# Optimization experiments

Measured on AMD Instinct MI355X. Metric: run time of the kernel, lower is better.

## Reference

```python
import jax, jax.numpy as jnp
import numpy as np
import math

PHI = (1 + math.sqrt(5)) / 2
COMPRESS_EXP = 2.0 / 3.0
ALPHA_D = 0.01


def c_mag(z):
    return jnp.sqrt(z[..., 0] ** 2 + z[..., 1] ** 2 + 1e-08)


def c_phase(z):
    return jnp.arctan2(z[..., 1], z[..., 0] + 1e-10)


def c_mul(a, b):
    real = a[..., 0] * b[..., 0] - a[..., 1] * b[..., 1]
    imag = a[..., 0] * b[..., 1] + a[..., 1] * b[..., 0]
    return jnp.stack([real, imag], axis=-1)


@jax.custom_vjp
def fractal_compress(mag):
    return jnp.clip(mag, 1e-08) ** COMPRESS_EXP


def _fc_fwd(mag):
    ms = jnp.clip(mag, 1e-08)
    c = ms ** COMPRESS_EXP
    return c, c / (ms + 1e-06)


def _fc_bwd(ratio, g):
    return (g * jnp.minimum(ratio, 2.0),)


fractal_compress.defvjp(_fc_fwd, _fc_bwd)


def converge(z):
    mag = c_mag(z)
    phase = c_phase(z)
    cm = fractal_compress(mag)
    return jnp.stack([cm * jnp.cos(phase), cm * jnp.sin(phase)], axis=-1)


def setup_inputs():
    key = jax.random.key(0)
    Bsz, T, D, S = 4, 512, 1024, 16
    dt_rank = D // 16
    ks = jax.random.split(key, 8)
    scale = 1.0 / PHI

    def u(k, shape):
        fan_in = shape[1]
        lim = scale / math.sqrt(fan_in)
        return jax.random.uniform(k, shape, minval=-lim, maxval=lim, dtype=jnp.float32)

    return {
        "x": jax.random.normal(ks[0], (Bsz, T, D), dtype=jnp.float32),
        "W_in": u(ks[1], (2 * D, D)),
        "W_xproj": u(ks[2], (dt_rank + 4 * S, D)),
        "W_dt": u(ks[3], (D, dt_rank)),
        "b_dt": jax.random.uniform(ks[4], (D,), minval=-0.1, maxval=0.1, dtype=jnp.float32),
        "W_out": u(ks[5], (D, D)),
        "b_out": jax.random.uniform(ks[6], (D,), minval=-0.1, maxval=0.1, dtype=jnp.float32),
        "W_res": u(ks[7], (2 * S, D)),
        "A_log": jnp.log(jnp.linspace(1.0, float(S), S)),
    }


def reference(x, W_in, W_xproj, W_dt, b_dt, W_out, b_out, W_res, A_log):
    Bsz, T, D = x.shape
    S = A_log.shape[0]
    dt_rank = W_dt.shape[1]

    xz = x @ W_in.T                      # [B,T,2D]
    x_in, z = xz[..., :D], xz[..., D:]
    x_in = jax.nn.silu(x_in)
    xp = x_in @ W_xproj.T                # [B,T,dt_rank+4S]
    dt = jax.nn.softplus(xp[..., :dt_rank] @ W_dt.T + b_dt)   # [B,T,D]
    bc = xp[..., dt_rank:].reshape(Bsz, T, 2, S, 2)
    B_all, C_all = bc[:, :, 0], bc[:, :, 1]                    # [B,T,S,2]

    A_neg = -jnp.exp(A_log)              # [S]

    # initial deep state d: differentiated phases, tiny magnitude
    phases = jnp.linspace(0.0, 2 * math.pi * (1 - 1.0 / S), S)
    d0 = jnp.stack([0.01 * jnp.cos(phases), 0.01 * jnp.sin(phases)], axis=-1)
    d0 = jnp.broadcast_to(d0, (Bsz, S, 2)).astype(x.dtype)
    h0 = jnp.zeros((Bsz, D, S, 2), dtype=x.dtype)

    def step(carry, xs):
        h_prev, d_prev = carry
        x_t, dt_t, B_t, C_t = xs        # [B,D], [B,D], [B,S,2], [B,S,2]
        x_complex = (x_t @ W_res.T).reshape(Bsz, S, 2)
        d_read = jax.lax.stop_gradient(d_prev)
        T_gate = jnp.cos((c_phase(x_complex) - c_phase(d_read)) / 2) ** 2  # [B,S]
        d_mag = c_mag(d_read)[..., None]
        d_normed = d_read / (d_mag + 1e-08)
        d_scale = jnp.sqrt(jnp.clip(d_mag, 1e-06, 20.0))
        surfaced = d_normed * d_scale * T_gate[..., None]                  # [B,S,2]

        alpha = jnp.exp(dt_t[..., None] * A_neg)                           # [B,D,S]
        x_full = jnp.stack([x_t, jnp.zeros_like(x_t)], axis=-1)            # [B,D,2]
        Bx = c_mul(B_t[:, None, :, :], x_full[:, :, None, :])              # [B,D,S,2]
        Bx = Bx + surfaced[:, None, :, :]
        Bx = Bx * dt_t[:, :, None, None]                                   # gamma scaling

        h_decayed = h_prev * alpha[..., None]
        released = h_prev * (1.0 - alpha)[..., None]
        comp = jnp.clip(converge(released), -10.0, 10.0)
        comp_avg = comp.mean(axis=1)                                       # [B,S,2]
        d_t = jax.lax.stop_gradient(d_prev) + ALPHA_D * comp_avg
        d_mag_new = c_mag(d_t)[..., None]
        d_t = jnp.where(d_mag_new > 20.0, d_t * (20.0 / d_mag_new), d_t)

        h_t = h_decayed + Bx
        Ch = c_mul(C_t[:, None, :, :], h_t)                                # [B,D,S,2]
        y_t = Ch[..., 0].sum(axis=-1)                                      # [B,D]
        return (h_t, d_t), y_t

    xs = (
        jnp.swapaxes(x_in, 0, 1),
        jnp.swapaxes(dt, 0, 1),
        jnp.swapaxes(B_all, 0, 1),
        jnp.swapaxes(C_all, 0, 1),
    )
    (_, _), ys = jax.lax.scan(step, (h0, d0), xs)
    y = jnp.swapaxes(ys, 0, 1)           # [B,T,D]
    y = y * jax.nn.silu(z)
    return y @ W_out.T + b_out
```

## Files before the change

kernel.cpp:

```cpp
#include <hip/hip_runtime.h>
#include <hip/hip_bf16.h>
#include <math.h>


enum { EPI_NONE=0, EPI_SILU=1, EPI_SPBIAS=2, EPI_BIAS=3 };

template<int EPI>
__device__ __forceinline__ float epi_apply(float v, float b) {
  if constexpr (EPI == EPI_SILU)        { return v / (1.0f + expf(-v)); }
  else if constexpr (EPI == EPI_SPBIAS) { float t = v + b; return fmaxf(t, 0.0f) + log1pf(expf(-fabsf(t))); }
  else if constexpr (EPI == EPI_BIAS)   { return v + b; }
  else return v;
}

template<int EPI, bool HAS_A2>
__global__ __launch_bounds__(256) void gemm_wt(
    const float* __restrict__ A, int lda,
    const float* __restrict__ A2, int lda2,
    const float* __restrict__ W, int ldw,
    const float* __restrict__ bias,
    float* __restrict__ C, int ldc,
    int N, int K)
{
  constexpr int BM = 64, BN = 64, BK = 16, PAD = 4;
  __shared__ float As[BK][BM + PAD];
  __shared__ float Ws[BK][BN + PAD];
  const int m0 = blockIdx.x * BM;
  const int n0 = blockIdx.y * BN;
  const int tid = threadIdx.x;
  const int tx = tid & 15;
  const int ty = tid >> 4;
  const int lm = tid >> 2;
  const int lk = (tid & 3) << 2;

  float acc[4][4] = {{0.f,0.f,0.f,0.f},{0.f,0.f,0.f,0.f},{0.f,0.f,0.f,0.f},{0.f,0.f,0.f,0.f}};

  for (int k0 = 0; k0 < K; k0 += BK) {
    float4 av, wv;
    {
      const float* p = A + (size_t)(m0 + lm) * lda + k0 + lk;
      av = *(const float4*)p;
      if (HAS_A2) {
        const float4 a2 = *(const float4*)(A2 + (size_t)(m0 + lm) * lda2 + k0 + lk);
        av.x *= a2.x; av.y *= a2.y; av.z *= a2.z; av.w *= a2.w;
      }
    }
    {
      const int n = n0 + lm;
      if (n < N) wv = *(const float4*)(W + (size_t)n * ldw + k0 + lk);
      else       wv = make_float4(0.f, 0.f, 0.f, 0.f);
    }
    __syncthreads();
    As[lk+0][lm] = av.x; As[lk+1][lm] = av.y; As[lk+2][lm] = av.z; As[lk+3][lm] = av.w;
    Ws[lk+0][lm] = wv.x; Ws[lk+1][lm] = wv.y; Ws[lk+2][lm] = wv.z; Ws[lk+3][lm] = wv.w;
    __syncthreads();
#pragma unroll
    for (int kk = 0; kk < BK; ++kk) {
      const float4 a = *(const float4*)&As[kk][ty << 2];
      const float4 w = *(const float4*)&Ws[kk][tx << 2];
      const float ar[4] = {a.x, a.y, a.z, a.w};
      const float wr[4] = {w.x, w.y, w.z, w.w};
#pragma unroll
      for (int i = 0; i < 4; ++i)
#pragma unroll
        for (int j = 0; j < 4; ++j)
          acc[i][j] = fmaf(ar[i], wr[j], acc[i][j]);
    }
  }

  const int ncol = n0 + (tx << 2);
  float bj[4] = {0.f, 0.f, 0.f, 0.f};
  if constexpr (EPI == EPI_SPBIAS || EPI == EPI_BIAS) {
    if (ncol < N) { const float4 bv = *(const float4*)(bias + ncol); bj[0]=bv.x; bj[1]=bv.y; bj[2]=bv.z; bj[3]=bv.w; }
  }
  if (ncol < N) {
#pragma unroll
    for (int i = 0; i < 4; ++i) {
      float vs[4];
#pragma unroll
      for (int j = 0; j < 4; ++j) vs[j] = epi_apply<EPI>(acc[i][j], bj[j]);
      *(float4*)(C + (size_t)(m0 + (ty << 2) + i) * ldc + ncol) = make_float4(vs[0], vs[1], vs[2], vs[3]);
    }
  }
}

__global__ __launch_bounds__(256) void gemm_dualw(
    const float* __restrict__ A, int lda,
    const float* __restrict__ W1,
    const float* __restrict__ W2, int ldw,
    float* __restrict__ C, int ldc,
    int N, int K)
{
  constexpr int BM = 64, BN = 64, BK = 16, PAD = 4;
  __shared__ float As[BK][BM + PAD];
  __shared__ float Ws[BK][BN + PAD];
  const int m0 = blockIdx.x * BM;
  const int n0 = blockIdx.y * BN;
  const int tid = threadIdx.x;
  const int tx = tid & 15;
  const int ty = tid >> 4;
  const int lm = tid >> 2;
  const int lk = (tid & 3) << 2;

  float acc[4][4] = {{0.f,0.f,0.f,0.f},{0.f,0.f,0.f,0.f},{0.f,0.f,0.f,0.f},{0.f,0.f,0.f,0.f}};

  for (int k0 = 0; k0 < K; k0 += BK) {
    float4 av, wv;
    av = *(const float4*)(A + (size_t)(m0 + lm) * lda + k0 + lk);
    {
      const int n = n0 + lm;
      if (n < N) {
        const float* wp = (n < 128) ? (W1 + (size_t)n * ldw + k0 + lk)
                                    : (W2 + (size_t)(n - 128) * ldw + k0 + lk);
        wv = *(const float4*)wp;
      } else wv = make_float4(0.f, 0.f, 0.f, 0.f);
    }
    __syncthreads();
    As[lk+0][lm] = av.x; As[lk+1][lm] = av.y; As[lk+2][lm] = av.z; As[lk+3][lm] = av.w;
    Ws[lk+0][lm] = wv.x; Ws[lk+1][lm] = wv.y; Ws[lk+2][lm] = wv.z; Ws[lk+3][lm] = wv.w;
    __syncthreads();
#pragma unroll
    for (int kk = 0; kk < BK; ++kk) {
      const float4 a = *(const float4*)&As[kk][ty << 2];
      const float4 w = *(const float4*)&Ws[kk][tx << 2];
      const float ar[4] = {a.x, a.y, a.z, a.w};
      const float wr[4] = {w.x, w.y, w.z, w.w};
#pragma unroll
      for (int i = 0; i < 4; ++i)
#pragma unroll
        for (int j = 0; j < 4; ++j)
          acc[i][j] = fmaf(ar[i], wr[j], acc[i][j]);
    }
  }

  const int ncol = n0 + (tx << 2);
  if (ncol < N) {
#pragma unroll
    for (int i = 0; i < 4; ++i)
      *(float4*)(C + (size_t)(m0 + (ty << 2) + i) * ldc + ncol) =
          make_float4(acc[i][0], acc[i][1], acc[i][2], acc[i][3]);
  }
}

template<int EPI>
__global__ __launch_bounds__(256) void gemm_128x64(
    const float* __restrict__ A, int lda,
    const float* __restrict__ W, int ldw,
    float* __restrict__ C, int ldc, int K)
{
  constexpr int BM = 128, BN = 64, BK = 16, PAD = 4;
  __shared__ float As[BK][BM + PAD];
  __shared__ float Ws[BK][BN + PAD];
  const int m0 = blockIdx.x * BM;
  const int n0 = blockIdx.y * BN;
  const int tid = threadIdx.x;
  const int tx = tid & 15;
  const int ty = tid >> 4;
  const int lmA = tid >> 1;
  const int lkA = (tid & 1) << 3;
  const int lmW = tid >> 2;
  const int lkW = (tid & 3) << 2;

  float acc[8][4];
#pragma unroll
  for (int i = 0; i < 8; ++i)
#pragma unroll
    for (int j = 0; j < 4; ++j) acc[i][j] = 0.f;

  for (int k0 = 0; k0 < K; k0 += BK) {
    const float* pa = A + (size_t)(m0 + lmA) * lda + k0 + lkA;
    const float4 a0 = ((const float4*)pa)[0];
    const float4 a1 = ((const float4*)pa)[1];
    const float4 wv = *(const float4*)(W + (size_t)(n0 + lmW) * ldw + k0 + lkW);
    __syncthreads();
    As[lkA+0][lmA]=a0.x; As[lkA+1][lmA]=a0.y; As[lkA+2][lmA]=a0.z; As[lkA+3][lmA]=a0.w;
    As[lkA+4][lmA]=a1.x; As[lkA+5][lmA]=a1.y; As[lkA+6][lmA]=a1.z; As[lkA+7][lmA]=a1.w;
    Ws[lkW+0][lmW]=wv.x; Ws[lkW+1][lmW]=wv.y; Ws[lkW+2][lmW]=wv.z; Ws[lkW+3][lmW]=wv.w;
    __syncthreads();
#pragma unroll
    for (int kk = 0; kk < BK; ++kk) {
      const float4 x0 = *(const float4*)&As[kk][ty << 3];
      const float4 x1 = *(const float4*)&As[kk][(ty << 3) + 4];
      const float4 w  = *(const float4*)&Ws[kk][tx << 2];
      const float ar[8] = {x0.x,x0.y,x0.z,x0.w,x1.x,x1.y,x1.z,x1.w};
      const float wr[4] = {w.x,w.y,w.z,w.w};
#pragma unroll
      for (int i = 0; i < 8; ++i)
#pragma unroll
        for (int j = 0; j < 4; ++j)
          acc[i][j] = fmaf(ar[i], wr[j], acc[i][j]);
    }
  }

  const int ncol = n0 + (tx << 2);
#pragma unroll
  for (int i = 0; i < 8; ++i) {
    float vs[4];
#pragma unroll
    for (int j = 0; j < 4; ++j) vs[j] = epi_apply<EPI>(acc[i][j], 0.f);
    *(float4*)(C + (size_t)(m0 + (ty << 3) + i) * ldc + ncol) = make_float4(vs[0], vs[1], vs[2], vs[3]);
  }
}

__global__ __launch_bounds__(256) void gemm_dt64(
    const float* __restrict__ A, int lda,
    const float* __restrict__ W,
    const float* __restrict__ bias,
    float* __restrict__ C, int ldc)
{
  __shared__ float As[64][68];
  __shared__ float Ws[64][68];
  const int m0 = blockIdx.x * 64;
  const int n0 = blockIdx.y * 64;
  const int tid = threadIdx.x;
  const int lm = tid & 63;
  const int kq = (tid >> 6) << 4;

  {
    const float* pa = A + (size_t)(m0 + lm) * lda + kq;
    const float4 a0 = ((const float4*)pa)[0];
    const float4 a1 = ((const float4*)pa)[1];
    const float4 a2 = ((const float4*)pa)[2];
    const float4 a3 = ((const float4*)pa)[3];
    const float* pw = W + (size_t)(n0 + lm) * 64 + kq;
    const float4 w0 = ((const float4*)pw)[0];
    const float4 w1 = ((const float4*)pw)[1];
    const float4 w2 = ((const float4*)pw)[2];
    const float4 w3 = ((const float4*)pw)[3];
    As[kq+ 0][lm]=a0.x; As[kq+ 1][lm]=a0.y; As[kq+ 2][lm]=a0.z; As[kq+ 3][lm]=a0.w;
    As[kq+ 4][lm]=a1.x; As[kq+ 5][lm]=a1.y; As[kq+ 6][lm]=a1.z; As[kq+ 7][lm]=a1.w;
    As[kq+ 8][lm]=a2.x; As[kq+ 9][lm]=a2.y; As[kq+10][lm]=a2.z; As[kq+11][lm]=a2.w;
    As[kq+12][lm]=a3.x; As[kq+13][lm]=a3.y; As[kq+14][lm]=a3.z; As[kq+15][lm]=a3.w;
    Ws[kq+ 0][lm]=w0.x; Ws[kq+ 1][lm]=w0.y; Ws[kq+ 2][lm]=w0.z; Ws[kq+ 3][lm]=w0.w;
    Ws[kq+ 4][lm]=w1.x; Ws[kq+ 5][lm]=w1.y; Ws[kq+ 6][lm]=w1.z; Ws[kq+ 7][lm]=w1.w;
    Ws[kq+ 8][lm]=w2.x; Ws[kq+ 9][lm]=w2.y; Ws[kq+10][lm]=w2.z; Ws[kq+11][lm]=w2.w;
    Ws[kq+12][lm]=w3.x; Ws[kq+13][lm]=w3.y; Ws[kq+14][lm]=w3.z; Ws[kq+15][lm]=w3.w;
  }
  __syncthreads();

  const int tx = tid & 15;
  const int ty = tid >> 4;
  float acc[4][4] = {{0.f,0.f,0.f,0.f},{0.f,0.f,0.f,0.f},{0.f,0.f,0.f,0.f},{0.f,0.f,0.f,0.f}};
#pragma unroll 16
  for (int kk = 0; kk < 64; ++kk) {
    const float4 a = *(const float4*)&As[kk][ty << 2];
    const float4 w = *(const float4*)&Ws[kk][tx << 2];
    const float ar[4] = {a.x, a.y, a.z, a.w};
    const float wr[4] = {w.x, w.y, w.z, w.w};
#pragma unroll
    for (int i = 0; i < 4; ++i)
#pragma unroll
      for (int j = 0; j < 4; ++j)
        acc[i][j] = fmaf(ar[i], wr[j], acc[i][j]);
  }

  const int ncol = n0 + (tx << 2);
  const float4 bv = *(const float4*)(bias + ncol);
  const float bj[4] = {bv.x, bv.y, bv.z, bv.w};
#pragma unroll
  for (int i = 0; i < 4; ++i) {
    float vs[4];
#pragma unroll
    for (int j = 0; j < 4; ++j) vs[j] = epi_apply<EPI_SPBIAS>(acc[i][j], bj[j]);
    *(float4*)(C + (size_t)(m0 + (ty << 2) + i) * ldc + ncol) = make_float4(vs[0], vs[1], vs[2], vs[3]);
  }
}

__global__ void zero_kernel(float4* __restrict__ p, int n4) {
  const int i = blockIdx.x * blockDim.x + threadIdx.x;
  if (i < n4) p[i] = make_float4(0.f, 0.f, 0.f, 0.f);
}

__global__ __launch_bounds__(256) void reduce_y(const float4* __restrict__ yp, float4* __restrict__ yo, int n4) {
  const int i = blockIdx.x * blockDim.x + threadIdx.x;
  if (i >= n4) return;
  float4 a = yp[i];
#pragma unroll
  for (int s = 1; s < 16; ++s) {
    const float4 v = yp[(size_t)s * 524288 + i];
    a.x += v.x; a.y += v.y; a.z += v.z; a.w += v.w;
  }
  yo[i] = a;
}

template<int CTRL>
__device__ __forceinline__ float dpp_fadd(float x) {
  const int s = __builtin_amdgcn_update_dpp(0, __float_as_int(x), CTRL, 0xF, 0xF, true);
  return x + __int_as_float(s);
}
__device__ __forceinline__ float wave64_sum_l63(float x) {
  x = dpp_fadd<0x111>(x);
  x = dpp_fadd<0x112>(x);
  x = dpp_fadd<0x114>(x);
  x = dpp_fadd<0x118>(x);
  x = dpp_fadd<0x142>(x);
  x = dpp_fadd<0x143>(x);
  return x;
}

__device__ __forceinline__ void comp_block(const float4& dtv, const float na2,
    const float (&h_r)[4], const float (&h_i)[4], float (&al_out)[4],
    float& wr, float& wi)
{
  const float ta[4] = {dtv.x, dtv.y, dtv.z, dtv.w};
  float sr = 0.f, si = 0.f;
#pragma unroll
  for (int e = 0; e < 4; ++e) {
    const float a = exp2f(ta[e] * na2);
    al_out[e] = a;
    const float om    = 1.0f - a;
    const float rel_r = h_r[e] * om, rel_i = h_i[e] * om;
    const float m2 = fmaf(rel_r, rel_r, fmaf(rel_i, rel_i, 1e-8f));
    const float u  = exp2f(log2f(m2) * (-1.0f / 6.0f));
    const float rr = rel_r + 1e-10f;
    float cr = rr * u;    cr = fminf(fmaxf(cr, -10.f), 10.f);
    float ci = rel_i * u; ci = fminf(fmaxf(ci, -10.f), 10.f);
    sr += cr; si += ci;
  }
  wr = wave64_sum_l63(sr);
  wi = wave64_sum_l63(si);
}

template<bool PARTIAL>
__device__ __forceinline__ void step_update(
    float& d_r, float& d_i, const float avg_r, const float avg_i,
    const float2& cx, const float4& xv, const float4& dtv,
    const float2& Bv, const float2& Cv,
    const float (&alv)[4], float (&h_r)[4], float (&h_i)[4],
    float* py)
{
  d_r = fmaf(0.01f, avg_r, d_r);
  d_i = fmaf(0.01f, avg_i, d_i);
  const float dm2c = fmaf(d_r, d_r, fmaf(d_i, d_i, 1e-8f));
  if (dm2c > 400.f) { const float sc = 20.f * __builtin_amdgcn_rsqf(dm2c); d_r *= sc; d_i *= sc; }

  const float xr2 = cx.x + 1e-10f;
  const float irx = __builtin_amdgcn_rsqf(fmaf(xr2, xr2, fmaf(cx.y, cx.y, 1e-38f)));
  const float dr2 = d_r + 1e-10f;
  const float ird = __builtin_amdgcn_rsqf(fmaf(dr2, dr2, fmaf(d_i, d_i, 1e-38f)));
  const float cosdp = fmaf(xr2, dr2, cx.y * d_i) * irx * ird;
  const float Tg  = 0.5f * (1.0f + cosdp);
  const float md2 = fmaf(d_r, d_r, fmaf(d_i, d_i, 1e-8f));
  const float sf  = Tg * exp2f(log2f(md2) * -0.25f);
  const float s_r = d_r * sf, s_i = d_i * sf;

  const float xa[4] = {xv.x, xv.y, xv.z, xv.w};
  const float ta[4] = {dtv.x, dtv.y, dtv.z, dtv.w};
  float yv[4];
#pragma unroll
  for (int e = 0; e < 4; ++e) {
    const float bx_r = fmaf(Bv.x, xa[e], s_r) * ta[e];
    const float bx_i = fmaf(Bv.y, xa[e], s_i) * ta[e];
    h_r[e] = fmaf(h_r[e], alv[e], bx_r);
    h_i[e] = fmaf(h_i[e], alv[e], bx_i);
    yv[e] = fmaf(Cv.x, h_r[e], -(Cv.y * h_i[e]));
  }
  if (PARTIAL) {
    *(float4*)py = make_float4(yv[0], yv[1], yv[2], yv[3]);
  } else {
#pragma unroll
    for (int e = 0; e < 4; ++e) atomicAdd(py + e, yv[e]);
  }
}

template<int RB, int RO, bool PARTIAL>
__device__ __forceinline__ void period_body(
    const float* __restrict__ px, const float* __restrict__ pdt,
    const float* __restrict__ pB, const float* __restrict__ pC,
    const float* __restrict__ pxc, float* __restrict__ py,
    const float na2, const int lane, const int wid,
    float (*red)[4][4],
    float& d_r, float& d_i,
    float (&h_r)[4], float (&h_i)[4], float (&al)[4],
    float4& x0, float4& t0, float2& B0, float2& C0, float2& c0,
    float4& x1, float4& t1, float2& B1, float2& C1, float2& c1,
    const float4& t2)
{
  const float4 qa = *(const float4*)&red[RB][0][0];
  const float4 qb = *(const float4*)&red[RB][1][0];
  const float4 qc = *(const float4*)&red[RB][2][0];
  const float4 qd = *(const float4*)&red[RB][3][0];

  step_update<PARTIAL>(d_r, d_i,
      (qa.x + qb.x + qc.x + qd.x) * (1.0f / 1024.0f),
      (qa.y + qb.y + qc.y + qd.y) * (1.0f / 1024.0f),
      c0, x0, t0, B0, C0, al, h_r, h_i, py + (size_t)RO * 1024);

  x0 = *(const float4*)(px  + (size_t)(RO + 3) * 2048);
  t0 = *(const float4*)(pdt + (size_t)(RO + 3) * 1024);
  B0 = *(const float2*)(pB  + (RO + 3) * 160);
  C0 = *(const float2*)(pC  + (RO + 3) * 160);
  c0 = *(const float2*)(pxc + (RO + 3) * 160);

  float al1[4], w1r, w1i;
  comp_block(t1, na2, h_r, h_i, al1, w1r, w1i);

  step_update<PARTIAL>(d_r, d_i,
      (qa.z + qb.z + qc.z + qd.z) * (1.0f / 1024.0f),
      (qa.w + qb.w + qc.w + qd.w) * (1.0f / 1024.0f),
      c1, x1, t1, B1, C1, al1, h_r, h_i, py + (size_t)(RO + 1) * 1024);

  x1 = *(const float4*)(px  + (size_t)(RO + 4) * 2048);
  t1 = *(const float4*)(pdt + (size_t)(RO + 4) * 1024);
  B1 = *(const float2*)(pB  + (RO + 4) * 160);
  C1 = *(const float2*)(pC  + (RO + 4) * 160);
  c1 = *(const float2*)(pxc + (RO + 4) * 160);

  float w2r, w2i;
  comp_block(t2, na2, h_r, h_i, al, w2r, w2i);

  if (lane == 63) *(float4*)&red[(RB + 1) % 3][wid][0] = make_float4(w1r, w1i, w2r, w2i);

  asm volatile("s_waitcnt lgkmcnt(0)" ::: "memory");
  __builtin_amdgcn_s_barrier();
  asm volatile("" ::: "memory");
}

template<bool PARTIAL>
__global__ __launch_bounds__(256) void scan_kernel(
    const float* __restrict__ xin,
    const float* __restrict__ xpc,
    const float* __restrict__ dtb,
    const float* __restrict__ A_log,
    float* __restrict__ ybase,
    int T)
{
  const int b = blockIdx.x >> 4;
  const int s = blockIdx.x & 15;
  const int d0 = threadIdx.x << 2;
  const int lane = threadIdx.x & 63;
  const int wid = threadIdx.x >> 6;

  __shared__ __align__(16) float red[3][4][4];

  const float a_s = expf(A_log[s]);
  const float na2 = -a_s * 1.4426950408889634f;
  const float phase = (float)(6.283185307179586 * (double)s / 16.0);
  float d_r = 0.01f * cosf(phase);
  float d_i = 0.01f * sinf(phase);
  float h_r[4] = {0.f,0.f,0.f,0.f};
  float h_i[4] = {0.f,0.f,0.f,0.f};
  float al[4];

  const size_t rb = (size_t)b * T;
  const float* px  = xin + rb * 2048 + d0;
  const float* pdt = dtb + rb * 1024 + d0;
  const float* pB  = xpc + rb * 160 + 64 + 2 * s;
  const float* pC  = xpc + rb * 160 + 96 + 2 * s;
  const float* pxc = xpc + rb * 160 + 128 + 2 * s;
  float* py = PARTIAL ? (ybase + (size_t)s * (4 * 512 * 1024) + rb * 1024 + d0)
                      : (ybase + rb * 1024 + d0);

  float4 xA = *(const float4*)px;
  float4 tA = *(const float4*)pdt;
  float2 BA = *(const float2*)pB;
  float2 CA = *(const float2*)pC;
  float2 cA = *(const float2*)pxc;
  float4 xB = *(const float4*)(px + 2048);
  float4 tB = *(const float4*)(pdt + 1024);
  float2 BB = *(const float2*)(pB + 160);
  float2 CB = *(const float2*)(pC + 160);
  float2 cB = *(const float2*)(pxc + 160);
  float4 xC = *(const float4*)(px + 2 * 2048);
  float4 tC = *(const float4*)(pdt + 2 * 1024);
  float2 BC = *(const float2*)(pB + 2 * 160);
  float2 CC = *(const float2*)(pC + 2 * 160);
  float2 cC = *(const float2*)(pxc + 2 * 160);

  {
    float w0r, w0i;
    comp_block(tA, na2, h_r, h_i, al, w0r, w0i);
    if (lane == 63) *(float4*)&red[0][wid][0] = make_float4(0.f, 0.f, w0r, w0i);
  }
  __syncthreads();

  for (int it = 0; it < 85; ++it) {
    period_body<0, 0, PARTIAL>(px, pdt, pB, pC, pxc, py, na2, lane, wid, red,
        d_r, d_i, h_r, h_i, al,
        xA, tA, BA, CA, cA,  xB, tB, BB, CB, cB,  tC);
    period_body<1, 2, PARTIAL>(px, pdt, pB, pC, pxc, py, na2, lane, wid, red,
        d_r, d_i, h_r, h_i, al,
        xC, tC, BC, CC, cC,  xA, tA, BA, CA, cA,  tB);
    period_body<2, 4, PARTIAL>(px, pdt, pB, pC, pxc, py, na2, lane, wid, red,
        d_r, d_i, h_r, h_i, al,
        xB, tB, BB, CB, cB,  xC, tC, BC, CC, cC,  tA);
    px += 6 * 2048; pdt += 6 * 1024; pB += 6 * 160; pC += 6 * 160; pxc += 6 * 160;
    py += 6 * 1024;
  }
  period_body<0, 0, PARTIAL>(px, pdt, pB, pC, pxc, py, na2, lane, wid, red,
      d_r, d_i, h_r, h_i, al,
      xA, tA, BA, CA, cA,  xB, tB, BB, CB, cB,  tC);
}

extern "C" void kernel_launch(void* const* d_in, const int* in_sizes, int n_in,
                              void* d_out, int out_size, void* d_ws, size_t ws_size,
                              hipStream_t stream) {
  const float* x     = (const float*)d_in[0];
  const float* W_in  = (const float*)d_in[1];
  const float* W_xp  = (const float*)d_in[2];
  const float* W_dt  = (const float*)d_in[3];
  const float* b_dt  = (const float*)d_in[4];
  const float* W_out = (const float*)d_in[5];
  const float* b_out = (const float*)d_in[6];
  const float* W_res = (const float*)d_in[7];
  const float* A_log = (const float*)d_in[8];
  float* out = (float*)d_out;

  float* ws     = (float*)d_ws;
  float* siluxz = ws;
  float* xpc    = siluxz + (size_t)2048 * 2048;
  float* dtb    = xpc    + (size_t)2048 * 160;
  float* ybuf   = dtb    + (size_t)2048 * 1024;
  float* ypart  = ybuf   + (size_t)2048 * 1024;

  const size_t need_bytes = ((size_t)8716288 + (size_t)33554432) * 4;
  const bool use_part = ws_size >= need_bytes;

  gemm_128x64<EPI_SILU><<<dim3(16, 32), 256, 0, stream>>>(
      x, 1024, W_in, 1024, siluxz, 2048, 1024);
  gemm_dualw<<<dim3(32, 3), 256, 0, stream>>>(
      siluxz, 2048, W_xp, W_res, 1024, xpc, 160, 160, 1024);
  gemm_dt64<<<dim3(32, 16), 256, 0, stream>>>(
      xpc, 160, W_dt, b_dt, dtb, 1024);

  if (use_part) {
    scan_kernel<true><<<dim3(64), dim3(256), 0, stream>>>(
        siluxz, xpc, dtb, A_log, ypart, 512);
    reduce_y<<<dim3(2048), 256, 0, stream>>>((const float4*)ypart, (float4*)ybuf, 524288);
  } else {
    zero_kernel<<<dim3(2048), 256, 0, stream>>>((float4*)ybuf, (2048 * 1024) / 4);
    scan_kernel<false><<<dim3(64), dim3(256), 0, stream>>>(
        siluxz, xpc, dtb, A_log, ybuf, 512);
  }

  gemm_wt<EPI_BIAS, true><<<dim3(32, 16), 256, 0, stream>>>(
      ybuf, 1024, siluxz + 1024, 2048, W_out, 1024, b_out, out, 1024, 1024, 1024);
}
```

Baseline: 557.2 us.

## Run scan with one wave per block, 16 channels per lane, no barriers

The scan kernel moves from 256 threads holding 4 channels each to a single 64-lane wave holding 16 channels each. The cross-wave shared-memory reduction and s_barrier per step are replaced by an in-wave DPP/readlane all-reduce, and the one-step-lagged d update is kept. This removes block-level synchronisation from the serial recurrence. In exchange each wave does four times more serial math per step, needs more registers, and only 64 waves run on the whole GPU, so latency hiding depends on ILP within a lane.

```diff
diff --git a/kernel.cpp b/kernel.cpp
--- a/kernel.cpp
+++ b/kernel.cpp
@@ -288,27 +288,44 @@
   const int s = __builtin_amdgcn_update_dpp(0, __float_as_int(x), CTRL, 0xF, 0xF, true);
   return x + __int_as_float(s);
 }
-__device__ __forceinline__ float wave64_sum_l63(float x) {
-  x = dpp_fadd<0x111>(x);
-  x = dpp_fadd<0x112>(x);
-  x = dpp_fadd<0x114>(x);
-  x = dpp_fadd<0x118>(x);
-  x = dpp_fadd<0x142>(x);
-  x = dpp_fadd<0x143>(x);
-  return x;
-}
-
-__device__ __forceinline__ void comp_block(const float4& dtv, const float na2,
-    const float (&h_r)[4], const float (&h_i)[4], float (&al_out)[4],
-    float& wr, float& wi)
-{
-  const float ta[4] = {dtv.x, dtv.y, dtv.z, dtv.w};
+__device__ __forceinline__ float wave_allsum(float x) {
+  x = dpp_fadd<0xB1>(x);
+  x = dpp_fadd<0x4E>(x);
+  x = dpp_fadd<0x141>(x);
+  x = dpp_fadd<0x140>(x);
+  const int xi = __float_as_int(x);
+  return __int_as_float(__builtin_amdgcn_readlane(xi, 0))
+       + __int_as_float(__builtin_amdgcn_readlane(xi, 16))
+       + __int_as_float(__builtin_amdgcn_readlane(xi, 32))
+       + __int_as_float(__builtin_amdgcn_readlane(xi, 48));
+}
+
+template<int J, bool PARTIAL>
+__device__ __forceinline__ void step64(
+    const float* __restrict__ px, const float* __restrict__ pdt,
+    const float* __restrict__ pB, const float* __restrict__ pC,
+    const float* __restrict__ pxc, float* __restrict__ py,
+    const float na2,
+    float& d_r, float& d_i, float& ps_r, float& ps_i,
+    float (&h_r)[16], float (&h_i)[16],
+    float4 (&xs)[2][4], float4 (&ts)[2][4],
+    float2 (&Bs)[2], float2 (&Cs)[2], float2 (&cs)[2])
+{
+  float ta[16], xa[16];
+#pragma unroll
+  for (int q = 0; q < 4; ++q) {
+    ta[4*q+0] = ts[J][q].x; ta[4*q+1] = ts[J][q].y; ta[4*q+2] = ts[J][q].z; ta[4*q+3] = ts[J][q].w;
+    xa[4*q+0] = xs[J][q].x; xa[4*q+1] = xs[J][q].y; xa[4*q+2] = xs[J][q].z; xa[4*q+3] = xs[J][q].w;
+  }
+  const float2 Bv = Bs[J], Cv = Cs[J], cx = cs[J];
+
+  float al[16];
   float sr = 0.f, si = 0.f;
 #pragma unroll
-  for (int e = 0; e < 4; ++e) {
+  for (int e = 0; e < 16; ++e) {
     const float a = exp2f(ta[e] * na2);
-    al_out[e] = a;
-    const float om    = 1.0f - a;
+    al[e] = a;
+    const float om = 1.0f - a;
     const float rel_r = h_r[e] * om, rel_i = h_i[e] * om;
     const float m2 = fmaf(rel_r, rel_r, fmaf(rel_i, rel_i, 1e-8f));
     const float u  = exp2f(log2f(m2) * (-1.0f / 6.0f));
@@ -317,23 +334,13 @@
     float ci = rel_i * u; ci = fminf(fmaxf(ci, -10.f), 10.f);
     sr += cr; si += ci;
   }
-  wr = wave64_sum_l63(sr);
-  wi = wave64_sum_l63(si);
-}
-
-template<bool PARTIAL>
-__device__ __forceinline__ void step_update(
-    float& d_r, float& d_i, const float avg_r, const float avg_i,
-    const float2& cx, const float4& xv, const float4& dtv,
-    const float2& Bv, const float2& Cv,
-    const float (&alv)[4], float (&h_r)[4], float (&h_i)[4],
-    float* py)
-{
-  d_r = fmaf(0.01f, avg_r, d_r);
-  d_i = fmaf(0.01f, avg_i, d_i);
+  const float S_r = wave_allsum(sr);
+  const float S_i = wave_allsum(si);
+
+  d_r = fmaf(0.01f, ps_r * (1.0f / 1024.0f), d_r);
+  d_i = fmaf(0.01f, ps_i * (1.0f / 1024.0f), d_i);
   const float dm2c = fmaf(d_r, d_r, fmaf(d_i, d_i, 1e-8f));
   if (dm2c > 400.f) { const float sc = 20.f * __builtin_amdgcn_rsqf(dm2c); d_r *= sc; d_i *= sc; }
-
   const float xr2 = cx.x + 1e-10f;
   const float irx = __builtin_amdgcn_rsqf(fmaf(xr2, xr2, fmaf(cx.y, cx.y, 1e-38f)));
   const float dr2 = d_r + 1e-10f;
@@ -344,80 +351,38 @@
   const float sf  = Tg * exp2f(log2f(md2) * -0.25f);
   const float s_r = d_r * sf, s_i = d_i * sf;
 
-  const float xa[4] = {xv.x, xv.y, xv.z, xv.w};
-  const float ta[4] = {dtv.x, dtv.y, dtv.z, dtv.w};
-  float yv[4];
-#pragma unroll
-  for (int e = 0; e < 4; ++e) {
+  float yv[16];
+#pragma unroll
+  for (int e = 0; e < 16; ++e) {
     const float bx_r = fmaf(Bv.x, xa[e], s_r) * ta[e];
     const float bx_i = fmaf(Bv.y, xa[e], s_i) * ta[e];
-    h_r[e] = fmaf(h_r[e], alv[e], bx_r);
-    h_i[e] = fmaf(h_i[e], alv[e], bx_i);
+    h_r[e] = fmaf(h_r[e], al[e], bx_r);
+    h_i[e] = fmaf(h_i[e], al[e], bx_i);
     yv[e] = fmaf(Cv.x, h_r[e], -(Cv.y * h_i[e]));
   }
   if (PARTIAL) {
-    *(float4*)py = make_float4(yv[0], yv[1], yv[2], yv[3]);
+#pragma unroll
+    for (int q = 0; q < 4; ++q)
+      *(float4*)(py + (size_t)J * 1024 + 4*q) =
+          make_float4(yv[4*q+0], yv[4*q+1], yv[4*q+2], yv[4*q+3]);
   } else {
 #pragma unroll
-    for (int e = 0; e < 4; ++e) atomicAdd(py + e, yv[e]);
-  }
-}
-
-template<int RB, int RO, bool PARTIAL>
-__device__ __forceinline__ void period_body(
-    const float* __restrict__ px, const float* __restrict__ pdt,
-    const float* __restrict__ pB, const float* __restrict__ pC,
-    const float* __restrict__ pxc, float* __restrict__ py,
-    const float na2, const int lane, const int wid,
-    float (*red)[4][4],
-    float& d_r, float& d_i,
-    float (&h_r)[4], float (&h_i)[4], float (&al)[4],
-    float4& x0, float4& t0, float2& B0, float2& C0, float2& c0,
-    float4& x1, float4& t1, float2& B1, float2& C1, float2& c1,
-    const float4& t2)
-{
-  const float4 qa = *(const float4*)&red[RB][0][0];
-  const float4 qb = *(const float4*)&red[RB][1][0];
-  const float4 qc = *(const float4*)&red[RB][2][0];
-  const float4 qd = *(const float4*)&red[RB][3][0];
-
-  step_update<PARTIAL>(d_r, d_i,
-      (qa.x + qb.x + qc.x + qd.x) * (1.0f / 1024.0f),
-      (qa.y + qb.y + qc.y + qd.y) * (1.0f / 1024.0f),
-      c0, x0, t0, B0, C0, al, h_r, h_i, py + (size_t)RO * 1024);
-
-  x0 = *(const float4*)(px  + (size_t)(RO + 3) * 2048);
-  t0 = *(const float4*)(pdt + (size_t)(RO + 3) * 1024);
-  B0 = *(const float2*)(pB  + (RO + 3) * 160);
-  C0 = *(const float2*)(pC  + (RO + 3) * 160);
-  c0 = *(const float2*)(pxc + (RO + 3) * 160);
-
-  float al1[4], w1r, w1i;
-  comp_block(t1, na2, h_r, h_i, al1, w1r, w1i);
-
-  step_update<PARTIAL>(d_r, d_i,
-      (qa.z + qb.z + qc.z + qd.z) * (1.0f / 1024.0f),
-      (qa.w + qb.w + qc.w + qd.w) * (1.0f / 1024.0f),
-      c1, x1, t1, B1, C1, al1, h_r, h_i, py + (size_t)(RO + 1) * 1024);
-
-  x1 = *(const float4*)(px  + (size_t)(RO + 4) * 2048);
-  t1 = *(const float4*)(pdt + (size_t)(RO + 4) * 1024);
-  B1 = *(const float2*)(pB  + (RO + 4) * 160);
-  C1 = *(const float2*)(pC  + (RO + 4) * 160);
-  c1 = *(const float2*)(pxc + (RO + 4) * 160);
-
-  float w2r, w2i;
-  comp_block(t2, na2, h_r, h_i, al, w2r, w2i);
-
-  if (lane == 63) *(float4*)&red[(RB + 1) % 3][wid][0] = make_float4(w1r, w1i, w2r, w2i);
-
-  asm volatile("s_waitcnt lgkmcnt(0)" ::: "memory");
-  __builtin_amdgcn_s_barrier();
-  asm volatile("" ::: "memory");
+    for (int e = 0; e < 16; ++e) atomicAdd(py + (size_t)J * 1024 + e, yv[e]);
+  }
+
+  ps_r = S_r; ps_i = S_i;
+#pragma unroll
+  for (int q = 0; q < 4; ++q) {
+    xs[J][q] = *(const float4*)(px  + (size_t)(J + 2) * 2048 + 4*q);
+    ts[J][q] = *(const float4*)(pdt + (size_t)(J + 2) * 1024 + 4*q);
+  }
+  Bs[J] = *(const float2*)(pB  + (J + 2) * 160);
+  Cs[J] = *(const float2*)(pC  + (J + 2) * 160);
+  cs[J] = *(const float2*)(pxc + (J + 2) * 160);
 }
 
 template<bool PARTIAL>
-__global__ __launch_bounds__(256) void scan_kernel(
+__global__ __launch_bounds__(64) void scan_kernel(
     const float* __restrict__ xin,
     const float* __restrict__ xpc,
     const float* __restrict__ dtb,
@@ -427,20 +392,17 @@
 {
   const int b = blockIdx.x >> 4;
   const int s = blockIdx.x & 15;
-  const int d0 = threadIdx.x << 2;
-  const int lane = threadIdx.x & 63;
-  const int wid = threadIdx.x >> 6;
-
-  __shared__ __align__(16) float red[3][4][4];
+  const int d0 = threadIdx.x << 4;
 
   const float a_s = expf(A_log[s]);
   const float na2 = -a_s * 1.4426950408889634f;
   const float phase = (float)(6.283185307179586 * (double)s / 16.0);
   float d_r = 0.01f * cosf(phase);
   float d_i = 0.01f * sinf(phase);
-  float h_r[4] = {0.f,0.f,0.f,0.f};
-  float h_i[4] = {0.f,0.f,0.f,0.f};
-  float al[4];
+  float h_r[16], h_i[16];
+#pragma unroll
+  for (int e = 0; e < 16; ++e) { h_r[e] = 0.f; h_i[e] = 0.f; }
+  float ps_r = 0.f, ps_i = 0.f;
 
   const size_t rb = (size_t)b * T;
   const float* px  = xin + rb * 2048 + d0;
@@ -451,45 +413,28 @@
   float* py = PARTIAL ? (ybase + (size_t)s * (4 * 512 * 1024) + rb * 1024 + d0)
                       : (ybase + rb * 1024 + d0);
 
-  float4 xA = *(const float4*)px;
-  float4 tA = *(const float4*)pdt;
-  float2 BA = *(const float2*)pB;
-  float2 CA = *(const float2*)pC;
-  float2 cA = *(const float2*)pxc;
-  float4 xB = *(const float4*)(px + 2048);
-  float4 tB = *(const float4*)(pdt + 1024);
-  float2 BB = *(const float2*)(pB + 160);
-  float2 CB = *(const float2*)(pC + 160);
-  float2 cB = *(const float2*)(pxc + 160);
-  float4 xC = *(const float4*)(px + 2 * 2048);
-  float4 tC = *(const float4*)(pdt + 2 * 1024);
-  float2 BC = *(const float2*)(pB + 2 * 160);
-  float2 CC = *(const float2*)(pC + 2 * 160);
-  float2 cC = *(const float2*)(pxc + 2 * 160);
-
-  {
-    float w0r, w0i;
-    comp_block(tA, na2, h_r, h_i, al, w0r, w0i);
-    if (lane == 63) *(float4*)&red[0][wid][0] = make_float4(0.f, 0.f, w0r, w0i);
-  }
-  __syncthreads();
-
-  for (int it = 0; it < 85; ++it) {
-    period_body<0, 0, PARTIAL>(px, pdt, pB, pC, pxc, py, na2, lane, wid, red,
-        d_r, d_i, h_r, h_i, al,
-        xA, tA, BA, CA, cA,  xB, tB, BB, CB, cB,  tC);
-    period_body<1, 2, PARTIAL>(px, pdt, pB, pC, pxc, py, na2, lane, wid, red,
-        d_r, d_i, h_r, h_i, al,
-        xC, tC, BC, CC, cC,  xA, tA, BA, CA, cA,  tB);
-    period_body<2, 4, PARTIAL>(px, pdt, pB, pC, pxc, py, na2, lane, wid, red,
-        d_r, d_i, h_r, h_i, al,
-        xB, tB, BB, CB, cB,  xC, tC, BC, CC, cC,  tA);
-    px += 6 * 2048; pdt += 6 * 1024; pB += 6 * 160; pC += 6 * 160; pxc += 6 * 160;
-    py += 6 * 1024;
-  }
-  period_body<0, 0, PARTIAL>(px, pdt, pB, pC, pxc, py, na2, lane, wid, red,
-      d_r, d_i, h_r, h_i, al,
-      xA, tA, BA, CA, cA,  xB, tB, BB, CB, cB,  tC);
+  float4 xs[2][4], ts[2][4];
+  float2 Bs[2], Cs[2], cs[2];
+#pragma unroll
+  for (int j = 0; j < 2; ++j) {
+#pragma unroll
+    for (int q = 0; q < 4; ++q) {
+      xs[j][q] = *(const float4*)(px  + (size_t)j * 2048 + 4*q);
+      ts[j][q] = *(const float4*)(pdt + (size_t)j * 1024 + 4*q);
+    }
+    Bs[j] = *(const float2*)(pB  + j * 160);
+    Cs[j] = *(const float2*)(pC  + j * 160);
+    cs[j] = *(const float2*)(pxc + j * 160);
+  }
+
+  for (int it = 0; it < 256; ++it) {
+    step64<0, PARTIAL>(px, pdt, pB, pC, pxc, py, na2,
+        d_r, d_i, ps_r, ps_i, h_r, h_i, xs, ts, Bs, Cs, cs);
+    step64<1, PARTIAL>(px, pdt, pB, pC, pxc, py, na2,
+        d_r, d_i, ps_r, ps_i, h_r, h_i, xs, ts, Bs, Cs, cs);
+    px += 2 * 2048; pdt += 2 * 1024; pB += 2 * 160; pC += 2 * 160; pxc += 2 * 160;
+    py += 2 * 1024;
+  }
 }
 
 extern "C" void kernel_launch(void* const* d_in, const int* in_sizes, int n_in,
@@ -524,12 +469,12 @@
       xpc, 160, W_dt, b_dt, dtb, 1024);
 
   if (use_part) {
-    scan_kernel<true><<<dim3(64), dim3(256), 0, stream>>>(
+    scan_kernel<true><<<dim3(64), dim3(64), 0, stream>>>(
         siluxz, xpc, dtb, A_log, ypart, 512);
     reduce_y<<<dim3(2048), 256, 0, stream>>>((const float4*)ypart, (float4*)ybuf, 524288);
   } else {
     zero_kernel<<<dim3(2048), 256, 0, stream>>>((float4*)ybuf, (2048 * 1024) / 4);
-    scan_kernel<false><<<dim3(64), dim3(256), 0, stream>>>(
+    scan_kernel<false><<<dim3(64), dim3(64), 0, stream>>>(
         siluxz, xpc, dtb, A_log, ybuf, 512);
   }
 
```

Result: slower. 974.6 us (+74.9%).
